# Kernel tuning notes

Measured on AMD Instinct MI355X. Metric: run time of the kernel, lower is better.

Reference implementation:

```python
import jax, jax.numpy as jnp
import numpy as np
import math

N_HEAD, D_HEAD, D_MODEL = 12, 64, 768
ATT_SPAN = 512            # max_position_embeddings // stride**block_index
SCALE_FACTOR = 3          # 1 + 2 (relative attention: content + c2p + p2c)
CLS_TOKENS = 1            # num_highway_cls_tokens + 1
INF = 1e6
LN_EPS = 1e-5
SCALE = 1.0 / (math.sqrt(D_HEAD) * math.sqrt(SCALE_FACTOR))


def setup_inputs() -> dict:
    key = jax.random.key(0)
    ks = jax.random.split(key, 10)
    B, S = 2, 2048
    lin = lambda k, shape: jax.random.normal(k, shape, dtype=jnp.float32) * 0.02
    return {
        "query": jax.random.normal(ks[0], (B, S, D_MODEL), dtype=jnp.float32),
        "attention_mask": jnp.ones((B, S), dtype=jnp.float32),
        "pos_key_embed": jax.random.normal(ks[1], (2 * ATT_SPAN, D_MODEL), dtype=jnp.float32),
        "pos_query_embed": jax.random.normal(ks[2], (2 * ATT_SPAN, D_MODEL), dtype=jnp.float32),
        "Wq": lin(ks[3], (N_HEAD * D_HEAD, D_MODEL)),
        "bq": jnp.zeros((N_HEAD * D_HEAD,), dtype=jnp.float32),
        "Wk": lin(ks[4], (N_HEAD * D_HEAD, D_MODEL)),
        "Wv": lin(ks[5], (D_MODEL, D_MODEL)),
        "bv": jnp.zeros((D_MODEL,), dtype=jnp.float32),
        "Wpq": lin(ks[6], (N_HEAD * D_HEAD, D_MODEL)),
        "bpq": jnp.zeros((N_HEAD * D_HEAD,), dtype=jnp.float32),
        "Wpk": lin(ks[7], (N_HEAD * D_HEAD, D_MODEL)),
        "r_w_bias": jax.random.normal(ks[8], (N_HEAD, D_HEAD), dtype=jnp.float32) * 0.02,
        "ln_gamma": jnp.ones((D_MODEL,), dtype=jnp.float32),
        "ln_beta": jnp.zeros((D_MODEL,), dtype=jnp.float32),
    }


def _forward(query, attention_mask, pos_key_embed, pos_query_embed,
             Wq, bq, Wk, Wv, bv, Wpq, bpq, Wpk, r_w_bias, ln_gamma, ln_beta):
    B, S, _ = query.shape
    # self-attention: key = value = query
    v = query @ Wv.T + bv                                             # v_head projection
    qh = (query @ Wq.T + bq).reshape(B, S, N_HEAD, D_HEAD)
    kh = (query @ Wk.T).reshape(B, S, N_HEAD, D_HEAD)
    vh = v.reshape(B, S, N_HEAD, D_MODEL // N_HEAD)
    qh = (qh + r_w_bias) * SCALE                                       # bias + scale fused into q

    content = jnp.einsum('bind,bjnd->bnij', qh, kh)                    # [B,n,S,S]

    # ---- disentangled relative-position bias (DeBERTa-style c2p + p2c) ----
    pos_k = (pos_key_embed @ Wpk.T).reshape(2 * ATT_SPAN, N_HEAD, D_HEAD).transpose(1, 0, 2)          # [n,2span,d]
    pos_q = (pos_query_embed @ Wpq.T + bpq).reshape(2 * ATT_SPAN, N_HEAD, D_HEAD).transpose(1, 0, 2)  # [n,2span,d]
    qbn = qh.transpose(0, 2, 1, 3)                                     # [B,n,S,d] (already scaled)
    kbn = kh.transpose(0, 2, 1, 3)
    rel = jnp.arange(S)[:, None] - jnp.arange(S)[None, :]              # [S,S] query - key

    # content -> position
    c2p = jnp.einsum('bnid,njd->bnij', qbn, pos_k)                     # [B,n,S,2span]
    c2p_idx = jnp.clip(rel + ATT_SPAN, 0, 2 * ATT_SPAN - 1)
    c2p_score = jnp.take_along_axis(c2p, c2p_idx[None, None], axis=-1) # [B,n,S,S]

    # position -> content
    p2c = jnp.einsum('bnjd,nid->bnji', kbn * (1.0 / math.sqrt(D_HEAD * SCALE_FACTOR)), pos_q)  # [B,n,S,2span]
    p2c_idx = jnp.clip(-rel + ATT_SPAN, 0, 2 * ATT_SPAN - 1)
    p2c_score = jnp.take_along_axis(p2c, p2c_idx[None, None], axis=-1).swapaxes(-1, -2)        # [B,n,S,S]

    bias = c2p_score + p2c_score
    # zero out bias on cls rows and cls columns (the padding/concat trick in the source)
    keep = (jnp.arange(S) >= CLS_TOKENS).astype(bias.dtype)
    bias = bias * (keep[:, None] * keep[None, :])

    score = content + bias
    score = score - INF * (1.0 - attention_mask[:, None, None, :])
    prob = jax.nn.softmax(score, axis=-1)                              # attention_dropout = 0.0

    attn_vec = jnp.einsum('bnij,bjnd->bind', prob, vh).reshape(B, S, D_MODEL)
    # fused residual + LayerNorm(attn_out)
    mu = attn_vec.mean(-1, keepdims=True)
    var = ((attn_vec - mu) ** 2).mean(-1, keepdims=True)
    ln = (attn_vec - mu) / jnp.sqrt(var + LN_EPS) * ln_gamma + ln_beta
    return query + ln


def reference(query, attention_mask, pos_key_embed, pos_query_embed,
              Wq, bq, Wk, Wv, bv, Wpq, bpq, Wpk, r_w_bias, ln_gamma, ln_beta):
    return _forward(query, attention_mask, pos_key_embed, pos_query_embed,
                    Wq, bq, Wk, Wv, bv, Wpq, bpq, Wpk, r_w_bias, ln_gamma, ln_beta)
```

## Files before the change

kernel.cpp:

```cpp
#include <hip/hip_runtime.h>
#include <math.h>

#define NB     2
#define SEQ    2048
#define NHEAD  12
#define DMODEL 768
#define SPAN2  1024
#define SCALEF 0.07216878364870323f

typedef unsigned short ushort;
typedef unsigned int   uint;
typedef __attribute__((ext_vector_type(8))) short  bh8;
typedef __attribute__((ext_vector_type(4))) float  f32x4;
typedef __attribute__((ext_vector_type(4))) unsigned short us4;

__device__ inline ushort f2bf(float x) {
    uint u = __builtin_bit_cast(uint, x);
    u += 0x7FFFu + ((u >> 16) & 1u);
    return (ushort)(u >> 16);
}
__device__ inline float b2f(ushort h) {
    uint u = ((uint)h) << 16;
    return __builtin_bit_cast(float, u);
}

__device__ __forceinline__ void gld16(const ushort* g, ushort* l) {
    __builtin_amdgcn_global_load_lds(
        (const __attribute__((address_space(1))) void*)g,
        (__attribute__((address_space(3))) void*)l, 16, 0, 0);
}

__device__ __forceinline__ bh8 ldsfrag(const ushort* tile, int row, int slot) {
    return *(const bh8*)((const char*)tile + row * 128 + (((slot ^ (row & 7)) << 4)));
}

struct CvtArgs {
    const float* src[8];
    ushort*      dst[8];
    int          n[8];
};

__global__ __launch_bounds__(256) void cvt_bf16(CvtArgs a)
{
    const int seg = blockIdx.y;
    const int i   = (blockIdx.x * 256 + threadIdx.x) * 8;
    if (i >= a.n[seg]) return;
    const float4* s = (const float4*)(a.src[seg] + i);
    const float4 x = s[0], y = s[1];
    bh8 o;
    o[0] = (short)f2bf(x.x); o[1] = (short)f2bf(x.y);
    o[2] = (short)f2bf(x.z); o[3] = (short)f2bf(x.w);
    o[4] = (short)f2bf(y.x); o[5] = (short)f2bf(y.y);
    o[6] = (short)f2bf(y.z); o[7] = (short)f2bf(y.w);
    *(bh8*)(a.dst[seg] + i) = o;
}

__global__ __launch_bounds__(256) void proj_qkv(
    const ushort* __restrict__ X,
    const ushort* __restrict__ Wq, const ushort* __restrict__ Wk,
    const ushort* __restrict__ Wv,
    const float* __restrict__ bq, const float* __restrict__ rwb,
    const float* __restrict__ bv,
    ushort* __restrict__ qh, ushort* __restrict__ kh, ushort* __restrict__ vht)
{
    __shared__ ushort Xs [64 * 64];
    __shared__ ushort Wqs[64 * 64];
    __shared__ ushort Wks[64 * 64];
    __shared__ ushort Wvs[64 * 64];
    const int r0 = blockIdx.x * 64;
    const int n  = blockIdx.y;
    const int c0 = n * 64;
    const int tid  = threadIdx.x;
    const int w    = tid >> 6;
    const int lane = tid & 63;
    const int lo   = lane & 15;
    const int hi8  = (lane >> 4) * 8;
    const int g4   = (lane >> 4) * 4;
    const int w16  = w * 16;
    const int r8   = lane >> 3;
    const int sl   = lane & 7;
    const int slotA = hi8 >> 3;

    f32x4 aq[4] = {}, ak[4] = {}, av[4] = {};
    for (int k0 = 0; k0 < DMODEL; k0 += 64) {
        #pragma unroll
        for (int i = 0; i < 2; ++i) {
            const int c = i * 4 + w;
            const int r = c * 8 + r8;
            const int s = sl ^ (r & 7);
            gld16(X  + (size_t)(r0 + r) * DMODEL + k0 + s * 8, Xs  + c * 512);
            gld16(Wq + (size_t)(c0 + r) * DMODEL + k0 + s * 8, Wqs + c * 512);
            gld16(Wk + (size_t)(c0 + r) * DMODEL + k0 + s * 8, Wks + c * 512);
            gld16(Wv + (size_t)(c0 + r) * DMODEL + k0 + s * 8, Wvs + c * 512);
        }
        __syncthreads();
        const bh8 a0 = ldsfrag(Xs, w16 + lo, slotA);
        const bh8 a1 = ldsfrag(Xs, w16 + lo, 4 + slotA);
        #pragma unroll
        for (int ct = 0; ct < 4; ++ct) {
            const int row = ct * 16 + lo;
            aq[ct] = __builtin_amdgcn_mfma_f32_16x16x32_bf16(a0, ldsfrag(Wqs, row, slotA),     aq[ct], 0, 0, 0);
            aq[ct] = __builtin_amdgcn_mfma_f32_16x16x32_bf16(a1, ldsfrag(Wqs, row, 4 + slotA), aq[ct], 0, 0, 0);
            ak[ct] = __builtin_amdgcn_mfma_f32_16x16x32_bf16(a0, ldsfrag(Wks, row, slotA),     ak[ct], 0, 0, 0);
            ak[ct] = __builtin_amdgcn_mfma_f32_16x16x32_bf16(a1, ldsfrag(Wks, row, 4 + slotA), ak[ct], 0, 0, 0);
            av[ct] = __builtin_amdgcn_mfma_f32_16x16x32_bf16(a0, ldsfrag(Wvs, row, slotA),     av[ct], 0, 0, 0);
            av[ct] = __builtin_amdgcn_mfma_f32_16x16x32_bf16(a1, ldsfrag(Wvs, row, 4 + slotA), av[ct], 0, 0, 0);
        }
        __syncthreads();
    }

    const int rbase = r0 + w16 + g4;
    const int bb  = rbase >> 11;
    const int rr0 = rbase & (SEQ - 1);
    #pragma unroll
    for (int ct = 0; ct < 4; ++ct) {
        const int d = ct * 16 + lo;
        const int c = c0 + d;
        const float bqv = bq[c] + rwb[c];
        const float bvv = bv[c];
        us4 o;
        #pragma unroll
        for (int reg = 0; reg < 4; ++reg) {
            const size_t rowi = ((size_t)bb * NHEAD + n) * SEQ + rr0 + reg;
            qh[rowi * 64 + d] = f2bf((aq[ct][reg] + bqv) * SCALEF);
            kh[rowi * 64 + d] = f2bf(ak[ct][reg]);
            o[reg] = f2bf(av[ct][reg] + bvv);
        }
        *(us4*)&vht[(((size_t)bb * NHEAD + n) * 64 + d) * SEQ + rr0] = o;
    }
}

__global__ __launch_bounds__(256) void proj_pos(
    const ushort* __restrict__ PKe, const ushort* __restrict__ PQe,
    const ushort* __restrict__ Wpk, const ushort* __restrict__ Wpq,
    const float* __restrict__ bpq,
    ushort* __restrict__ pkp, ushort* __restrict__ pqp)
{
    __shared__ ushort Xk [32 * 64];
    __shared__ ushort Xq [32 * 64];
    __shared__ ushort Wks[64 * 64];
    __shared__ ushort Wqs[64 * 64];
    const int r0 = blockIdx.x * 32;
    const int n  = blockIdx.y;
    const int c0 = n * 64;
    const int tid  = threadIdx.x;
    const int w    = tid >> 6;
    const int lane = tid & 63;
    const int lo   = lane & 15;
    const int hi8  = (lane >> 4) * 8;
    const int g4   = (lane >> 4) * 4;
    const int wr   = w & 1;
    const int wc   = w >> 1;
    const int r8   = lane >> 3;
    const int sl   = lane & 7;
    const int slotA = hi8 >> 3;

    f32x4 apk[2] = {}, apq[2] = {};
    for (int k0 = 0; k0 < DMODEL; k0 += 64) {
        {
            const int r = w * 8 + r8;
            const int s = sl ^ (r & 7);
            gld16(PKe + (size_t)(r0 + r) * DMODEL + k0 + s * 8, Xk + w * 512);
            gld16(PQe + (size_t)(r0 + r) * DMODEL + k0 + s * 8, Xq + w * 512);
        }
        #pragma unroll
        for (int i = 0; i < 2; ++i) {
            const int c = i * 4 + w;
            const int r = c * 8 + r8;
            const int s = sl ^ (r & 7);
            gld16(Wpk + (size_t)(c0 + r) * DMODEL + k0 + s * 8, Wks + c * 512);
            gld16(Wpq + (size_t)(c0 + r) * DMODEL + k0 + s * 8, Wqs + c * 512);
        }
        __syncthreads();
        const bh8 xk0 = ldsfrag(Xk, wr * 16 + lo, slotA);
        const bh8 xk1 = ldsfrag(Xk, wr * 16 + lo, 4 + slotA);
        const bh8 xq0 = ldsfrag(Xq, wr * 16 + lo, slotA);
        const bh8 xq1 = ldsfrag(Xq, wr * 16 + lo, 4 + slotA);
        #pragma unroll
        for (int ct = 0; ct < 2; ++ct) {
            const int row = wc * 32 + ct * 16 + lo;
            apk[ct] = __builtin_amdgcn_mfma_f32_16x16x32_bf16(xk0, ldsfrag(Wks, row, slotA),     apk[ct], 0, 0, 0);
            apk[ct] = __builtin_amdgcn_mfma_f32_16x16x32_bf16(xk1, ldsfrag(Wks, row, 4 + slotA), apk[ct], 0, 0, 0);
            apq[ct] = __builtin_amdgcn_mfma_f32_16x16x32_bf16(xq0, ldsfrag(Wqs, row, slotA),     apq[ct], 0, 0, 0);
            apq[ct] = __builtin_amdgcn_mfma_f32_16x16x32_bf16(xq1, ldsfrag(Wqs, row, 4 + slotA), apq[ct], 0, 0, 0);
        }
        __syncthreads();
    }

    const int rr0 = r0 + wr * 16 + g4;
    #pragma unroll
    for (int ct = 0; ct < 2; ++ct) {
        const int d = wc * 32 + ct * 16 + lo;
        const int c = c0 + d;
        const float badd = bpq[c];
        #pragma unroll
        for (int reg = 0; reg < 4; ++reg) {
            const size_t rowi = ((size_t)n * SPAN2 + rr0 + reg);
            pkp[rowi * 64 + d] = f2bf(apk[ct][reg]);
            pqp[rowi * 64 + d] = f2bf((apq[ct][reg] + badd) * SCALEF);
        }
    }
}

__global__ __launch_bounds__(256) void cd_vec(
    const ushort* __restrict__ qh, const ushort* __restrict__ kh,
    const ushort* __restrict__ posk, const ushort* __restrict__ posq,
    float* __restrict__ cdv)
{
    __shared__ float pr[4][64];
    const int bn = blockIdx.y;
    const int n  = bn % NHEAD;
    const int tid = threadIdx.x;
    if (tid < 64) {
        pr[0][tid] = b2f(posk[((size_t)n * SPAN2) * 64 + tid]);
        pr[1][tid] = b2f(posk[((size_t)n * SPAN2 + SPAN2 - 1) * 64 + tid]);
        pr[2][tid] = b2f(posq[((size_t)n * SPAN2) * 64 + tid]);
        pr[3][tid] = b2f(posq[((size_t)n * SPAN2 + SPAN2 - 1) * 64 + tid]);
    }
    __syncthreads();
    const int row = blockIdx.x * 32 + (tid >> 3);
    const int e0  = (tid & 7) * 8;
    const bh8 q8 = *(const bh8*)&qh[((size_t)bn * SEQ + row) * 64 + e0];
    const bh8 k8 = *(const bh8*)&kh[((size_t)bn * SEQ + row) * 64 + e0];
    float a0 = 0.f, a1 = 0.f, a2 = 0.f, a3 = 0.f;
    #pragma unroll
    for (int t = 0; t < 8; ++t) {
        const float qv = b2f((ushort)q8[t]);
        const float kv = b2f((ushort)k8[t]);
        a0 += qv * pr[0][e0 + t];
        a1 += qv * pr[1][e0 + t];
        a2 += kv * pr[2][e0 + t];
        a3 += kv * pr[3][e0 + t];
    }
    #pragma unroll
    for (int off = 1; off <= 4; off <<= 1) {
        a0 += __shfl_xor(a0, off);
        a1 += __shfl_xor(a1, off);
        a2 += __shfl_xor(a2, off);
        a3 += __shfl_xor(a3, off);
    }
    if ((tid & 7) == 0) {
        cdv[((size_t)0 * NB * NHEAD + bn) * SEQ + row] = a0;
        cdv[((size_t)1 * NB * NHEAD + bn) * SEQ + row] = a1;
        cdv[((size_t)2 * NB * NHEAD + bn) * SEQ + row] = a2;
        cdv[((size_t)3 * NB * NHEAD + bn) * SEQ + row] = a3;
    }
}

__global__ __launch_bounds__(256, 3) void attn_mfma10(
    const ushort* __restrict__ qh, const ushort* __restrict__ kh,
    const ushort* __restrict__ vht, const ushort* __restrict__ posk,
    const ushort* __restrict__ posq, const float* __restrict__ mask,
    const float* __restrict__ cdv, float* __restrict__ attn)
{
    __shared__ ushort POS[128 * 64];
    __shared__ ushort Kb [64 * 64];
    __shared__ ushort Vb [64 * 64];
    __shared__ ushort T1c[64 * 68];
    __shared__ ushort T2c[64 * 68];

    const int id   = blockIdx.x;
    const int xcd  = id & 7;
    const int slot = id >> 3;
    const int bn   = xcd * 3 + (slot >> 5);
    const int i0   = (slot & 31) * 64;
    const int b    = bn / NHEAD;
    const int n    = bn % NHEAD;

    const int tid  = threadIdx.x;
    const int w    = tid >> 6;
    const int lane = tid & 63;
    const int lo   = lane & 15;
    const int hi8  = (lane >> 4) * 8;
    const int g4   = (lane >> 4) * 4;
    const int w16  = w * 16;
    const int r8   = lane >> 3;
    const int sl   = lane & 7;
    const int slotA = hi8 >> 3;

    const ushort* qrow = qh + ((size_t)bn * SEQ + i0 + w16 + lo) * 64;
    const bh8 qa0 = *(const bh8*)&qrow[hi8];
    const bh8 qa1 = *(const bh8*)&qrow[32 + hi8];

    const ushort* khb = kh   + (size_t)bn * SEQ * 64;
    const ushort* vtb = vht  + (size_t)bn * 64 * SEQ;
    const ushort* pkh = posk + (size_t)n * SPAN2 * 64;
    const ushort* pqh = posq + (size_t)n * SPAN2 * 64;
    const float*  mrw = mask + (size_t)b * SEQ;

    float C0r[4], C1r[4];
    {
        const float* C0p = cdv + (size_t)bn * SEQ;
        const float* C1p = cdv + ((size_t)NB * NHEAD + bn) * SEQ;
        #pragma unroll
        for (int reg = 0; reg < 4; ++reg) {
            C0r[reg] = C0p[i0 + w16 + g4 + reg];
            C1r[reg] = C1p[i0 + w16 + g4 + reg];
        }
    }
    const float* D0p = cdv + ((size_t)2 * NB * NHEAD + bn) * SEQ;
    const float* D1p = cdv + ((size_t)3 * NB * NHEAD + bn) * SEQ;

    f32x4 accPV[4] = {};
    float mrow[4] = {-1e30f, -1e30f, -1e30f, -1e30f};
    float lrow[4] = {0.f, 0.f, 0.f, 0.f};

    for (int j0 = 0; j0 < SEQ; j0 += 64) {
        const int d0base = i0 - j0 + 449;
        const bool clamp0 = (d0base <= -126);
        const bool clamp1 = (d0base >= 1023);

        if (!clamp0 && !clamp1) {
        #pragma unroll
        for (int i = 0; i < 2; ++i) {
            const int c = i * 4 + w;
            const int r = c * 8 + r8;
            const int s = sl ^ (r & 7);
            gld16(khb + (size_t)(j0 + r) * 64 + s * 8, Kb + c * 512);
        }
        #pragma unroll
        for (int i = 0; i < 4; ++i) {
            const int c = i * 4 + w;
            const int r = c * 8 + r8;
            const int s = sl ^ (r & 7);
            int gr = d0base + r; gr = gr < 0 ? 0 : (gr > SPAN2 - 1 ? SPAN2 - 1 : gr);
            gld16(pkh + (size_t)gr * 64 + s * 8, POS + c * 512);
        }
        __syncthreads();

        const bh8 ka0 = ldsfrag(Kb, w16 + lo, slotA);
        const bh8 ka1 = ldsfrag(Kb, w16 + lo, 4 + slotA);
        f32x4 z1[5];
        #pragma unroll
        for (int q = 0; q < 5; ++q) {
            const int u1 = (w + q) * 16 + lo;
            const bh8 pk0 = ldsfrag(POS, u1, slotA);
            const bh8 pk1 = ldsfrag(POS, u1, 4 + slotA);
            f32x4 a = {};
            a = __builtin_amdgcn_mfma_f32_16x16x32_bf16(qa0, pk0, a, 0, 0, 0);
            z1[q] = __builtin_amdgcn_mfma_f32_16x16x32_bf16(qa1, pk1, a, 0, 0, 0);
        }
        __syncthreads();

        #pragma unroll
        for (int i = 0; i < 4; ++i) {
            const int c = i * 4 + w;
            const int r = c * 8 + r8;
            const int s = sl ^ (r & 7);
            int gr = d0base + r; gr = gr < 0 ? 0 : (gr > SPAN2 - 1 ? SPAN2 - 1 : gr);
            gld16(pqh + (size_t)gr * 64 + s * 8, POS + c * 512);
        }
        #pragma unroll
        for (int i = 0; i < 2; ++i) {
            const int c = i * 4 + w;
            const int r = c * 8 + r8;
            const int s = sl ^ (r & 7);
            gld16(vtb + (size_t)r * SEQ + j0 + s * 8, Vb + c * 512);
        }
        #pragma unroll
        for (int q = 0; q < 5; ++q)
            #pragma unroll
            for (int reg = 0; reg < 4; ++reg) {
                const int cc2 = q * 16 + lo - g4 - reg;
                if (cc2 >= 0 && cc2 < 64)
                    T1c[(w16 + g4 + reg) * 68 + cc2] = f2bf(z1[q][reg]);
            }
        f32x4 accS[4];
        #pragma unroll
        for (int ct = 0; ct < 4; ++ct) {
            const bh8 kb0 = ldsfrag(Kb, ct * 16 + lo, slotA);
            const bh8 kb1 = ldsfrag(Kb, ct * 16 + lo, 4 + slotA);
            f32x4 z = {};
            z = __builtin_amdgcn_mfma_f32_16x16x32_bf16(qa0, kb0, z, 0, 0, 0);
            accS[ct] = __builtin_amdgcn_mfma_f32_16x16x32_bf16(qa1, kb1, z, 0, 0, 0);
        }
        float maskadd[4];
        #pragma unroll
        for (int ct = 0; ct < 4; ++ct)
            maskadd[ct] = -1e6f * (1.f - mrw[j0 + ct * 16 + lo]);
        __syncthreads();

        #pragma unroll
        for (int q = 0; q < 5; ++q) {
            const int u2 = (3 - w + q) * 16 + lo;
            const bh8 pq0 = ldsfrag(POS, u2, slotA);
            const bh8 pq1 = ldsfrag(POS, u2, 4 + slotA);
            f32x4 z = {};
            z = __builtin_amdgcn_mfma_f32_16x16x32_bf16(ka0, pq0, z, 0, 0, 0);
            z = __builtin_amdgcn_mfma_f32_16x16x32_bf16(ka1, pq1, z, 0, 0, 0);
            #pragma unroll
            for (int reg = 0; reg < 4; ++reg) {
                const int il2 = q * 16 + lo + g4 + reg - 15;
                if (il2 >= 0 && il2 < 64)
                    T2c[(w16 + g4 + reg) * 68 + il2] = f2bf(z[reg]);
            }
        }
        __syncthreads();

        float corr[4];
        char* pbase = (char*)POS + w * 2048;
        #pragma unroll
        for (int reg = 0; reg < 4; ++reg) {
            const int il = w16 + g4 + reg;
            const int gi = i0 + il;
            float s[4], rmax = -1e30f;
            #pragma unroll
            for (int ct = 0; ct < 4; ++ct) {
                const int jl = ct * 16 + lo;
                float v = accS[ct][reg];
                if (gi >= 1 && (j0 + jl) >= 1)
                    v += b2f(T1c[il * 68 + 63 - jl]) + b2f(T2c[jl * 68 + il]);
                v += maskadd[ct];
                s[ct] = v;
                rmax = fmaxf(rmax, v);
            }
            rmax = fmaxf(rmax, __shfl_xor(rmax, 1));
            rmax = fmaxf(rmax, __shfl_xor(rmax, 2));
            rmax = fmaxf(rmax, __shfl_xor(rmax, 4));
            rmax = fmaxf(rmax, __shfl_xor(rmax, 8));
            const float mnew = fmaxf(mrow[reg], rmax);
            const float cc   = __expf(mrow[reg] - mnew);
            float psum = 0.f;
            const int prow = g4 + reg;
            #pragma unroll
            for (int ct = 0; ct < 4; ++ct) {
                const float p = __expf(s[ct] - mnew);
                psum += p;
                *(ushort*)(pbase + prow * 128 + ((((ct * 16 + lo) * 2)) ^ ((prow & 7) * 16))) = f2bf(p);
            }
            psum += __shfl_xor(psum, 1);
            psum += __shfl_xor(psum, 2);
            psum += __shfl_xor(psum, 4);
            psum += __shfl_xor(psum, 8);
            lrow[reg] = lrow[reg] * cc + psum;
            mrow[reg] = mnew;
            corr[reg] = cc;
        }

        {
            const bh8 pa0 = *(const bh8*)(pbase + lo * 128 + ((slotA << 4) ^ ((lo & 7) * 16)));
            const bh8 pa1 = *(const bh8*)(pbase + lo * 128 + (((4 + slotA) << 4) ^ ((lo & 7) * 16)));
            #pragma unroll
            for (int dt = 0; dt < 4; ++dt) {
                const bh8 vb0 = ldsfrag(Vb, dt * 16 + lo, slotA);
                const bh8 vb1 = ldsfrag(Vb, dt * 16 + lo, 4 + slotA);
                f32x4 a = accPV[dt];
                #pragma unroll
                for (int reg = 0; reg < 4; ++reg) a[reg] *= corr[reg];
                a = __builtin_amdgcn_mfma_f32_16x16x32_bf16(pa0, vb0, a, 0, 0, 0);
                accPV[dt] = __builtin_amdgcn_mfma_f32_16x16x32_bf16(pa1, vb1, a, 0, 0, 0);
            }
        }
        __syncthreads();

        } else {
        const float* Dp = clamp0 ? D0p : D1p;
        float Dvv[4];
        #pragma unroll
        for (int ct = 0; ct < 4; ++ct)
            Dvv[ct] = Dp[j0 + ct * 16 + lo];
        float maskadd[4];
        #pragma unroll
        for (int ct = 0; ct < 4; ++ct)
            maskadd[ct] = -1e6f * (1.f - mrw[j0 + ct * 16 + lo]);

        #pragma unroll
        for (int i = 0; i < 2; ++i) {
            const int c = i * 4 + w;
            const int r = c * 8 + r8;
            const int s = sl ^ (r & 7);
            gld16(khb + (size_t)(j0 + r) * 64 + s * 8, Kb + c * 512);
            gld16(vtb + (size_t)r * SEQ + j0 + s * 8, Vb + c * 512);
        }
        __syncthreads();

        f32x4 accS[4];
        #pragma unroll
        for (int ct = 0; ct < 4; ++ct) {
            const bh8 kb0 = ldsfrag(Kb, ct * 16 + lo, slotA);
            const bh8 kb1 = ldsfrag(Kb, ct * 16 + lo, 4 + slotA);
            f32x4 z = {};
            z = __builtin_amdgcn_mfma_f32_16x16x32_bf16(qa0, kb0, z, 0, 0, 0);
            accS[ct] = __builtin_amdgcn_mfma_f32_16x16x32_bf16(qa1, kb1, z, 0, 0, 0);
        }

        float corr[4];
        char* pbase = (char*)POS + w * 2048;
        #pragma unroll
        for (int reg = 0; reg < 4; ++reg) {
            const int il = w16 + g4 + reg;
            const int gi = i0 + il;
            const float Cvv = clamp0 ? C0r[reg] : C1r[reg];
            float s[4], rmax = -1e30f;
            #pragma unroll
            for (int ct = 0; ct < 4; ++ct) {
                const int jl = ct * 16 + lo;
                float v = accS[ct][reg];
                if (gi >= 1 && (j0 + jl) >= 1)
                    v += Cvv + Dvv[ct];
                v += maskadd[ct];
                s[ct] = v;
                rmax = fmaxf(rmax, v);
            }
            rmax = fmaxf(rmax, __shfl_xor(rmax, 1));
            rmax = fmaxf(rmax, __shfl_xor(rmax, 2));
            rmax = fmaxf(rmax, __shfl_xor(rmax, 4));
            rmax = fmaxf(rmax, __shfl_xor(rmax, 8));
            const float mnew = fmaxf(mrow[reg], rmax);
            const float cc   = __expf(mrow[reg] - mnew);
            float psum = 0.f;
            const int prow = g4 + reg;
            #pragma unroll
            for (int ct = 0; ct < 4; ++ct) {
                const float p = __expf(s[ct] - mnew);
                psum += p;
                *(ushort*)(pbase + prow * 128 + ((((ct * 16 + lo) * 2)) ^ ((prow & 7) * 16))) = f2bf(p);
            }
            psum += __shfl_xor(psum, 1);
            psum += __shfl_xor(psum, 2);
            psum += __shfl_xor(psum, 4);
            psum += __shfl_xor(psum, 8);
            lrow[reg] = lrow[reg] * cc + psum;
            mrow[reg] = mnew;
            corr[reg] = cc;
        }

        {
            const bh8 pa0 = *(const bh8*)(pbase + lo * 128 + ((slotA << 4) ^ ((lo & 7) * 16)));
            const bh8 pa1 = *(const bh8*)(pbase + lo * 128 + (((4 + slotA) << 4) ^ ((lo & 7) * 16)));
            #pragma unroll
            for (int dt = 0; dt < 4; ++dt) {
                const bh8 vb0 = ldsfrag(Vb, dt * 16 + lo, slotA);
                const bh8 vb1 = ldsfrag(Vb, dt * 16 + lo, 4 + slotA);
                f32x4 a = accPV[dt];
                #pragma unroll
                for (int reg = 0; reg < 4; ++reg) a[reg] *= corr[reg];
                a = __builtin_amdgcn_mfma_f32_16x16x32_bf16(pa0, vb0, a, 0, 0, 0);
                accPV[dt] = __builtin_amdgcn_mfma_f32_16x16x32_bf16(pa1, vb1, a, 0, 0, 0);
            }
        }
        __syncthreads();
        }
    }

    #pragma unroll
    for (int reg = 0; reg < 4; ++reg) {
        const int i = i0 + w16 + g4 + reg;
        const float inv = 1.f / lrow[reg];
        #pragma unroll
        for (int dt = 0; dt < 4; ++dt)
            attn[((size_t)b * SEQ + i) * DMODEL + n * 64 + dt * 16 + lo] =
                accPV[dt][reg] * inv;
    }
}

__global__ __launch_bounds__(256) void resid_ln(
    float* __restrict__ attn, const float* __restrict__ query,
    const float* __restrict__ gamma, const float* __restrict__ beta)
{
    const int b = blockIdx.y;
    const int i = blockIdx.x;
    const size_t base = ((size_t)b * SEQ + i) * DMODEL;
    const int tid = threadIdx.x;

    float x[3];
    #pragma unroll
    for (int s = 0; s < 3; ++s) x[s] = attn[base + s * 256 + tid];

    float sum = x[0] + x[1] + x[2];
    float sq  = x[0]*x[0] + x[1]*x[1] + x[2]*x[2];
    #pragma unroll
    for (int off = 32; off; off >>= 1) {
        sum += __shfl_xor(sum, off);
        sq  += __shfl_xor(sq, off);
    }
    __shared__ float red[2][4];
    const int w = tid >> 6;
    if ((tid & 63) == 0) { red[0][w] = sum; red[1][w] = sq; }
    __syncthreads();
    sum = red[0][0] + red[0][1] + red[0][2] + red[0][3];
    sq  = red[1][0] + red[1][1] + red[1][2] + red[1][3];

    const float mu  = sum * (1.f / DMODEL);
    const float var = sq * (1.f / DMODEL) - mu * mu;
    const float inv = rsqrtf(var + 1e-5f);

    #pragma unroll
    for (int s = 0; s < 3; ++s) {
        const int c = s * 256 + tid;
        attn[base + c] = query[base + c] + (x[s] - mu) * inv * gamma[c] + beta[c];
    }
}

extern "C" void kernel_launch(void* const* d_in, const int* in_sizes, int n_in,
                              void* d_out, int out_size, void* d_ws, size_t ws_size,
                              hipStream_t stream)
{
    const float* query = (const float*)d_in[0];
    const float* mask  = (const float*)d_in[1];
    const float* pke   = (const float*)d_in[2];
    const float* pqe   = (const float*)d_in[3];
    const float* Wq    = (const float*)d_in[4];
    const float* bq    = (const float*)d_in[5];
    const float* Wk    = (const float*)d_in[6];
    const float* Wv    = (const float*)d_in[7];
    const float* bv    = (const float*)d_in[8];
    const float* Wpq   = (const float*)d_in[9];
    const float* bpq   = (const float*)d_in[10];
    const float* Wpk   = (const float*)d_in[11];
    const float* rwb   = (const float*)d_in[12];
    const float* gamma = (const float*)d_in[13];
    const float* beta  = (const float*)d_in[14];

    float* out = (float*)d_out;

    const int Q_N  = NB * SEQ * DMODEL;
    const int P_N  = SPAN2 * DMODEL;
    const int W_N  = DMODEL * DMODEL;
    const size_t QKV_ELEMS = (size_t)NB * NHEAD * SEQ * 64;
    const size_t POS_ELEMS = (size_t)NHEAD * SPAN2 * 64;

    ushort* xb   = (ushort*)d_ws;
    ushort* pkeb = xb   + Q_N;
    ushort* pqeb = pkeb + P_N;
    ushort* wqb  = pqeb + P_N;
    ushort* wkb  = wqb  + W_N;
    ushort* wvb  = wkb  + W_N;
    ushort* wpqb = wvb  + W_N;
    ushort* wpkb = wpqb + W_N;
    ushort* qh   = wpkb + W_N;
    ushort* kh   = qh   + QKV_ELEMS;
    ushort* vht  = kh   + QKV_ELEMS;
    ushort* pkp  = vht  + QKV_ELEMS;
    ushort* pqp  = pkp  + POS_ELEMS;
    float*  cdv  = (float*)(pqp + POS_ELEMS);

    dim3 blk(256);

    CvtArgs ca;
    ca.src[0] = query; ca.dst[0] = xb;   ca.n[0] = Q_N;
    ca.src[1] = pke;   ca.dst[1] = pkeb; ca.n[1] = P_N;
    ca.src[2] = pqe;   ca.dst[2] = pqeb; ca.n[2] = P_N;
    ca.src[3] = Wq;    ca.dst[3] = wqb;  ca.n[3] = W_N;
    ca.src[4] = Wk;    ca.dst[4] = wkb;  ca.n[4] = W_N;
    ca.src[5] = Wv;    ca.dst[5] = wvb;  ca.n[5] = W_N;
    ca.src[6] = Wpq;   ca.dst[6] = wpqb; ca.n[6] = W_N;
    ca.src[7] = Wpk;   ca.dst[7] = wpkb; ca.n[7] = W_N;
    cvt_bf16<<<dim3((Q_N / 8 + 255) / 256, 8), blk, 0, stream>>>(ca);

    proj_qkv<<<dim3(NB * SEQ / 64, NHEAD), blk, 0, stream>>>(
        xb, wqb, wkb, wvb, bq, rwb, bv, qh, kh, vht);
    proj_pos<<<dim3(SPAN2 / 32, NHEAD), blk, 0, stream>>>(
        pkeb, pqeb, wpkb, wpqb, bpq, pkp, pqp);

    cd_vec<<<dim3(SEQ / 32, NB * NHEAD), blk, 0, stream>>>(
        qh, kh, pkp, pqp, cdv);

    attn_mfma10<<<dim3(NB * NHEAD * (SEQ / 64)), blk, 0, stream>>>(
        qh, kh, vht, pkp, pqp, mask, cdv, out);

    resid_ln<<<dim3(SEQ, NB), blk, 0, stream>>>(out, query, gamma, beta);
}
```

Before: 207.9 us.

## Process two clamped key tiles per barrier in attention fast path

Result: slower. 230.6 us (+11.0%).

```diff
diff --git a/kernel.cpp b/kernel.cpp
--- a/kernel.cpp
+++ b/kernel.cpp
@@ -247,7 +247,7 @@
     }
 }
 
-__global__ __launch_bounds__(256, 3) void attn_mfma10(
+__global__ __launch_bounds__(256, 3) void attn_mfma13(
     const ushort* __restrict__ qh, const ushort* __restrict__ kh,
     const ushort* __restrict__ vht, const ushort* __restrict__ posk,
     const ushort* __restrict__ posq, const float* __restrict__ mask,
@@ -305,7 +305,8 @@
     float mrow[4] = {-1e30f, -1e30f, -1e30f, -1e30f};
     float lrow[4] = {0.f, 0.f, 0.f, 0.f};
 
-    for (int j0 = 0; j0 < SEQ; j0 += 64) {
+    int j0 = 0;
+    while (j0 < SEQ) {
         const int d0base = i0 - j0 + 449;
         const bool clamp0 = (d0base <= -126);
         const bool clamp1 = (d0base >= 1023);
@@ -452,17 +453,17 @@
             }
         }
         __syncthreads();
+        j0 += 64;
 
         } else {
-        const float* Dp = clamp0 ? D0p : D1p;
-        float Dvv[4];
-        #pragma unroll
-        for (int ct = 0; ct < 4; ++ct)
-            Dvv[ct] = Dp[j0 + ct * 16 + lo];
-        float maskadd[4];
-        #pragma unroll
-        for (int ct = 0; ct < 4; ++ct)
-            maskadd[ct] = -1e6f * (1.f - mrw[j0 + ct * 16 + lo]);
+        const int j0B = j0 + 64;
+        bool clamp0B = false, clamp1B = false;
+        if (j0B < SEQ) {
+            const int dB = i0 - j0B + 449;
+            clamp0B = (dB <= -126);
+            clamp1B = (dB >= 1023);
+        }
+        const bool pairB = clamp0B || clamp1B;
 
         #pragma unroll
         for (int i = 0; i < 2; ++i) {
@@ -472,60 +473,76 @@
             gld16(khb + (size_t)(j0 + r) * 64 + s * 8, Kb + c * 512);
             gld16(vtb + (size_t)r * SEQ + j0 + s * 8, Vb + c * 512);
         }
-        __syncthreads();
-
-        f32x4 accS[4];
-        #pragma unroll
-        for (int ct = 0; ct < 4; ++ct) {
-            const bh8 kb0 = ldsfrag(Kb, ct * 16 + lo, slotA);
-            const bh8 kb1 = ldsfrag(Kb, ct * 16 + lo, 4 + slotA);
-            f32x4 z = {};
-            z = __builtin_amdgcn_mfma_f32_16x16x32_bf16(qa0, kb0, z, 0, 0, 0);
-            accS[ct] = __builtin_amdgcn_mfma_f32_16x16x32_bf16(qa1, kb1, z, 0, 0, 0);
-        }
-
-        float corr[4];
-        char* pbase = (char*)POS + w * 2048;
-        #pragma unroll
-        for (int reg = 0; reg < 4; ++reg) {
-            const int il = w16 + g4 + reg;
-            const int gi = i0 + il;
-            const float Cvv = clamp0 ? C0r[reg] : C1r[reg];
-            float s[4], rmax = -1e30f;
+        if (pairB) {
+            #pragma unroll
+            for (int i = 0; i < 2; ++i) {
+                const int c = i * 4 + w;
+                const int r = c * 8 + r8;
+                const int s = sl ^ (r & 7);
+                gld16(khb + (size_t)(j0B + r) * 64 + s * 8, POS + c * 512);
+                gld16(vtb + (size_t)r * SEQ + j0B + s * 8, POS + 4096 + c * 512);
+            }
+        }
+        __syncthreads();
+
+        char* pbase = (char*)T1c + w * 2048;
+
+        {
+            const float* Dp = clamp0 ? D0p : D1p;
+            float Dvv[4], maskadd[4];
             #pragma unroll
             for (int ct = 0; ct < 4; ++ct) {
-                const int jl = ct * 16 + lo;
-                float v = accS[ct][reg];
-                if (gi >= 1 && (j0 + jl) >= 1)
-                    v += Cvv + Dvv[ct];
-                v += maskadd[ct];
-                s[ct] = v;
-                rmax = fmaxf(rmax, v);
-            }
-            rmax = fmaxf(rmax, __shfl_xor(rmax, 1));
-            rmax = fmaxf(rmax, __shfl_xor(rmax, 2));
-            rmax = fmaxf(rmax, __shfl_xor(rmax, 4));
-            rmax = fmaxf(rmax, __shfl_xor(rmax, 8));
-            const float mnew = fmaxf(mrow[reg], rmax);
-            const float cc   = __expf(mrow[reg] - mnew);
-            float psum = 0.f;
-            const int prow = g4 + reg;
+                Dvv[ct]     = Dp[j0 + ct * 16 + lo];
+                maskadd[ct] = -1e6f * (1.f - mrw[j0 + ct * 16 + lo]);
+            }
+            f32x4 accS[4];
             #pragma unroll
             for (int ct = 0; ct < 4; ++ct) {
-                const float p = __expf(s[ct] - mnew);
-                psum += p;
-                *(ushort*)(pbase + prow * 128 + ((((ct * 16 + lo) * 2)) ^ ((prow & 7) * 16))) = f2bf(p);
-            }
-            psum += __shfl_xor(psum, 1);
-            psum += __shfl_xor(psum, 2);
-            psum += __shfl_xor(psum, 4);
-            psum += __shfl_xor(psum, 8);
-            lrow[reg] = lrow[reg] * cc + psum;
-            mrow[reg] = mnew;
-            corr[reg] = cc;
-        }
-
-        {
+                const bh8 kb0 = ldsfrag(Kb, ct * 16 + lo, slotA);
+                const bh8 kb1 = ldsfrag(Kb, ct * 16 + lo, 4 + slotA);
+                f32x4 z = {};
+                z = __builtin_amdgcn_mfma_f32_16x16x32_bf16(qa0, kb0, z, 0, 0, 0);
+                accS[ct] = __builtin_amdgcn_mfma_f32_16x16x32_bf16(qa1, kb1, z, 0, 0, 0);
+            }
+            float corr[4];
+            #pragma unroll
+            for (int reg = 0; reg < 4; ++reg) {
+                const int il = w16 + g4 + reg;
+                const int gi = i0 + il;
+                const float Cvv = clamp0 ? C0r[reg] : C1r[reg];
+                float s[4], rmax = -1e30f;
+                #pragma unroll
+                for (int ct = 0; ct < 4; ++ct) {
+                    const int jl = ct * 16 + lo;
+                    float v = accS[ct][reg];
+                    if (gi >= 1 && (j0 + jl) >= 1)
+                        v += Cvv + Dvv[ct];
+                    v += maskadd[ct];
+                    s[ct] = v;
+                    rmax = fmaxf(rmax, v);
+                }
+                rmax = fmaxf(rmax, __shfl_xor(rmax, 1));
+                rmax = fmaxf(rmax, __shfl_xor(rmax, 2));
+                rmax = fmaxf(rmax, __shfl_xor(rmax, 4));
+                rmax = fmaxf(rmax, __shfl_xor(rmax, 8));
+                const float mnew = fmaxf(mrow[reg], rmax);
+                const float cc   = __expf(mrow[reg] - mnew);
+                float psum = 0.f;
+                const int prow = g4 + reg;
+                #pragma unroll
+                for (int ct = 0; ct < 4; ++ct) {
+                    const float p = __expf(s[ct] - mnew);
+                    psum += p;
+                    *(ushort*)(pbase + prow * 128 + ((((ct * 16 + lo) * 2)) ^ ((prow & 7) * 16))) = f2bf(p);
+                }
+                psum += __shfl_xor(psum, 1);
+                psum += __shfl_xor(psum, 2);
+                psum += __shfl_xor(psum, 4);
+                psum += __shfl_xor(psum, 8);
+                lrow[reg] = lrow[reg] * cc + psum;
+                mrow[reg] = mnew;
+                corr[reg] = cc;
+            }
             const bh8 pa0 = *(const bh8*)(pbase + lo * 128 + ((slotA << 4) ^ ((lo & 7) * 16)));
             const bh8 pa1 = *(const bh8*)(pbase + lo * 128 + (((4 + slotA) << 4) ^ ((lo & 7) * 16)));
             #pragma unroll
@@ -539,7 +556,80 @@
                 accPV[dt] = __builtin_amdgcn_mfma_f32_16x16x32_bf16(pa1, vb1, a, 0, 0, 0);
             }
         }
-        __syncthreads();
+
+        if (pairB) {
+            const ushort* Kb2 = POS;
+            const ushort* Vb2 = POS + 4096;
+            const float* Dp = clamp0B ? D0p : D1p;
+            float Dvv[4], maskadd[4];
+            #pragma unroll
+            for (int ct = 0; ct < 4; ++ct) {
+                Dvv[ct]     = Dp[j0B + ct * 16 + lo];
+                maskadd[ct] = -1e6f * (1.f - mrw[j0B + ct * 16 + lo]);
+            }
+            f32x4 accS[4];
+            #pragma unroll
+            for (int ct = 0; ct < 4; ++ct) {
+                const bh8 kb0 = ldsfrag(Kb2, ct * 16 + lo, slotA);
+                const bh8 kb1 = ldsfrag(Kb2, ct * 16 + lo, 4 + slotA);
+                f32x4 z = {};
+                z = __builtin_amdgcn_mfma_f32_16x16x32_bf16(qa0, kb0, z, 0, 0, 0);
+                accS[ct] = __builtin_amdgcn_mfma_f32_16x16x32_bf16(qa1, kb1, z, 0, 0, 0);
+            }
+            float corr[4];
+            #pragma unroll
+            for (int reg = 0; reg < 4; ++reg) {
+                const int il = w16 + g4 + reg;
+                const int gi = i0 + il;
+                const float Cvv = clamp0B ? C0r[reg] : C1r[reg];
+                float s[4], rmax = -1e30f;
+                #pragma unroll
+                for (int ct = 0; ct < 4; ++ct) {
+                    const int jl = ct * 16 + lo;
+                    float v = accS[ct][reg];
+                    if (gi >= 1 && (j0B + jl) >= 1)
+                        v += Cvv + Dvv[ct];
+                    v += maskadd[ct];
+                    s[ct] = v;
+                    rmax = fmaxf(rmax, v);
+                }
+                rmax = fmaxf(rmax, __shfl_xor(rmax, 1));
+                rmax = fmaxf(rmax, __shfl_xor(rmax, 2));
+                rmax = fmaxf(rmax, __shfl_xor(rmax, 4));
+                rmax = fmaxf(rmax, __shfl_xor(rmax, 8));
+                const float mnew = fmaxf(mrow[reg], rmax);
+                const float cc   = __expf(mrow[reg] - mnew);
+                float psum = 0.f;
+                const int prow = g4 + reg;
+                #pragma unroll
+                for (int ct = 0; ct < 4; ++ct) {
+                    const float p = __expf(s[ct] - mnew);
+                    psum += p;
+                    *(ushort*)(pbase + prow * 128 + ((((ct * 16 + lo) * 2)) ^ ((prow & 7) * 16))) = f2bf(p);
+                }
+                psum += __shfl_xor(psum, 1);
+                psum += __shfl_xor(psum, 2);
+                psum += __shfl_xor(psum, 4);
+                psum += __shfl_xor(psum, 8);
+                lrow[reg] = lrow[reg] * cc + psum;
+                mrow[reg] = mnew;
+                corr[reg] = cc;
+            }
+            const bh8 pa0 = *(const bh8*)(pbase + lo * 128 + ((slotA << 4) ^ ((lo & 7) * 16)));
+            const bh8 pa1 = *(const bh8*)(pbase + lo * 128 + (((4 + slotA) << 4) ^ ((lo & 7) * 16)));
+            #pragma unroll
+            for (int dt = 0; dt < 4; ++dt) {
+                const bh8 vb0 = ldsfrag(Vb2, dt * 16 + lo, slotA);
+                const bh8 vb1 = ldsfrag(Vb2, dt * 16 + lo, 4 + slotA);
+                f32x4 a = accPV[dt];
+                #pragma unroll
+                for (int reg = 0; reg < 4; ++reg) a[reg] *= corr[reg];
+                a = __builtin_amdgcn_mfma_f32_16x16x32_bf16(pa0, vb0, a, 0, 0, 0);
+                accPV[dt] = __builtin_amdgcn_mfma_f32_16x16x32_bf16(pa1, vb1, a, 0, 0, 0);
+            }
+        }
+        __syncthreads();
+        j0 += pairB ? 128 : 64;
         }
     }
 
@@ -656,7 +746,7 @@
     cd_vec<<<dim3(SEQ / 32, NB * NHEAD), blk, 0, stream>>>(
         qh, kh, pkp, pqp, cdv);
 
-    attn_mfma10<<<dim3(NB * NHEAD * (SEQ / 64)), blk, 0, stream>>>(
+    attn_mfma13<<<dim3(NB * NHEAD * (SEQ / 64)), blk, 0, stream>>>(
         qh, kh, vht, pkp, pqp, mask, cdv, out);
 
     resid_ln<<<dim3(SEQ, NB), blk, 0, stream>>>(out, query, gamma, beta);
```
